# Kernel optimization log

Measured on AMD Instinct MI355X. Metric: run time of the kernel, lower is better.

Reference implementation:

```python
import jax, jax.numpy as jnp
import numpy as np

K_TOP = 2  # top-k experts per token


def setup_inputs() -> dict:
    key = jax.random.key(0)
    k1, k2, k3 = jax.random.split(key, 3)
    B, S, H, E = 4, 2048, 1024, 8
    hidden_states = jax.random.normal(k1, (B, S, H), dtype=jnp.float32)
    router_w = jax.random.normal(k2, (E, H), dtype=jnp.float32) * 0.02
    expert_weights = jax.random.normal(k3, (E, H, H), dtype=jnp.float32) * 0.02
    return {"hidden_states": hidden_states, "router_w": router_w, "expert_weights": expert_weights}


def reference(hidden_states, router_w, expert_weights):
    B, S, H = hidden_states.shape
    x = hidden_states.reshape(-1, H)                      # [N, H], N = B*S
    logits = x @ router_w.T                               # [N, E]
    probs = jax.nn.softmax(logits, axis=-1)               # [N, E]
    topk_vals, topk_idx = jax.lax.top_k(probs, K_TOP)     # [N, K]
    topk_w = topk_vals / (topk_vals.sum(-1, keepdims=True) + 1e-6)  # [N, K]

    # Dense per-expert GEMM over all tokens (single-device dispatch = identity)
    expert_out = jnp.einsum('nh,eho->eno', x, expert_weights)  # [E, N, H]

    # all_to_all_combine: gather each token's K expert outputs
    combined = jnp.take_along_axis(
        expert_out.transpose(1, 0, 2),                    # [N, E, H]
        topk_idx[:, :, None], axis=1)                     # [N, K, H]
    combined = combined.transpose(1, 0, 2)                # [K, N, H]

    # remap bias: sum over last dim of one-hot(topk_idx) * router_prob == gathered prob
    remap_bias = jnp.take_along_axis(probs, topk_idx, axis=1).T[:, :, None]  # [K, N, 1]

    weights = topk_w.T[:, :, None]                        # [K, N, 1]
    out = ((combined + remap_bias) * weights).sum(axis=0) # [N, H]
    return out.reshape(B, S, H)
```

## Files before the change

### kernel.cpp

```cpp
#include <hip/hip_runtime.h>
#include <cstdint>

typedef unsigned short u16;
typedef __attribute__((ext_vector_type(8))) short short8;
typedef __attribute__((ext_vector_type(4))) float float4v;

#define NTOK 8192
#define HDIM 1024
#define NEXP 8
#define TM 128
#define TN 128
#define BK 32
#define MAXT 136

__device__ __forceinline__ u16 f2bf(float f) {
    union { float f; uint32_t u; } v; v.f = f;
    uint32_t u = v.u;
    return (u16)((u + 0x7FFFu + ((u >> 16) & 1u)) >> 16);
}

__device__ __forceinline__ void gll16(const u16* g, u16* l) {
    __builtin_amdgcn_global_load_lds(
        (const __attribute__((address_space(1))) uint32_t*)g,
        (__attribute__((address_space(3))) uint32_t*)l,
        16, 0, 0);
}

__global__ __launch_bounds__(256) void prep_w(const float* __restrict__ w,
                                              u16* __restrict__ wt) {
    __shared__ float tile[32][33];
    const int e  = blockIdx.z;
    const int k0 = blockIdx.x * 32;
    const int n0 = blockIdx.y * 32;
    const int r = threadIdx.x >> 3;
    const int c = (threadIdx.x & 7) * 4;
    const float4 v = *(const float4*)(w + ((size_t)e << 20) + (size_t)(k0 + r) * HDIM + n0 + c);
    tile[r][c] = v.x; tile[r][c+1] = v.y; tile[r][c+2] = v.z; tile[r][c+3] = v.w;
    __syncthreads();
    ushort4 o;
    o.x = f2bf(tile[c][r]); o.y = f2bf(tile[c+1][r]);
    o.z = f2bf(tile[c+2][r]); o.w = f2bf(tile[c+3][r]);
    *(ushort4*)(wt + ((size_t)e << 20) + (size_t)(n0 + r) * HDIM + k0 + c) = o;
}

__global__ __launch_bounds__(256) void router(const float* __restrict__ x,
                                              const float* __restrict__ rw,
                                              u16* __restrict__ x_bf,
                                              float* __restrict__ wt0,
                                              float* __restrict__ wt1,
                                              float* __restrict__ biasv,
                                              int* __restrict__ sel) {
    const int wv = threadIdx.x >> 6;
    const int l  = threadIdx.x & 63;
    const int n  = blockIdx.x * 4 + wv;
    const float4* xr = (const float4*)(x + (size_t)n * HDIM);
    ushort4* xo = (ushort4*)(x_bf + (size_t)n * HDIM);

    float4 xv[4];
#pragma unroll
    for (int t = 0; t < 4; t++) {
        xv[t] = xr[t * 64 + l];
        ushort4 p;
        p.x = f2bf(xv[t].x); p.y = f2bf(xv[t].y);
        p.z = f2bf(xv[t].z); p.w = f2bf(xv[t].w);
        xo[t * 64 + l] = p;
    }

    float logits[NEXP];
#pragma unroll
    for (int e = 0; e < NEXP; e++) {
        const float4* rwe = (const float4*)(rw + e * HDIM);
        float acc = 0.f;
#pragma unroll
        for (int t = 0; t < 4; t++) {
            const float4 r = rwe[t * 64 + l];
            acc += xv[t].x * r.x + xv[t].y * r.y + xv[t].z * r.z + xv[t].w * r.w;
        }
#pragma unroll
        for (int s = 32; s > 0; s >>= 1) acc += __shfl_xor(acc, s, 64);
        logits[e] = acc;
    }

    if (l == 0) {
        float mx = logits[0];
#pragma unroll
        for (int e = 1; e < NEXP; e++) mx = fmaxf(mx, logits[e]);
        float p[NEXP]; float sum = 0.f;
#pragma unroll
        for (int e = 0; e < NEXP; e++) { p[e] = expf(logits[e] - mx); sum += p[e]; }
        const float inv = 1.f / sum;
#pragma unroll
        for (int e = 0; e < NEXP; e++) p[e] *= inv;
        int e0 = 0;
#pragma unroll
        for (int e = 1; e < NEXP; e++) if (p[e] > p[e0]) e0 = e;
        int e1 = (e0 == 0) ? 1 : 0;
#pragma unroll
        for (int e = 0; e < NEXP; e++) if (e != e0 && p[e] > p[e1]) e1 = e;
        const float p0 = p[e0], p1 = p[e1];
        const float wsum = p0 + p1 + 1e-6f;
        const float w0 = p0 / wsum, w1 = p1 / wsum;
        wt0[n] = w0; wt1[n] = w1;
        biasv[n] = w0 * p0 + w1 * p1;
        sel[n] = e0 | (e1 << 8);
    }
}

__global__ __launch_bounds__(256) void build_lists(const int* __restrict__ sel,
                                                   int* __restrict__ lists,
                                                   int* __restrict__ counts) {
    const int n  = blockIdx.x * 256 + threadIdx.x;
    const int wv = threadIdx.x >> 6;
    const int l  = threadIdx.x & 63;
    const int s  = sel[n];
    const int e0 = s & 0xFF, e1 = s >> 8;
    __shared__ int wcnt[NEXP][4];
    __shared__ int ebase[NEXP];
    int pf0 = 0, pf1 = 0;
    const unsigned long long ltmask = (1ULL << l) - 1ULL;
#pragma unroll
    for (int e = 0; e < NEXP; e++) {
        const int slot = (e0 == e) ? 0 : ((e1 == e) ? 1 : -1);
        const unsigned long long bal = __ballot(slot >= 0);
        const int pf = __popcll(bal & ltmask);
        if (slot == 0) pf0 = pf;
        if (slot == 1) pf1 = pf;
        if (l == 0) wcnt[e][wv] = __popcll(bal);
    }
    __syncthreads();
    if (threadIdx.x < NEXP) {
        const int e = threadIdx.x;
        const int tot = wcnt[e][0] + wcnt[e][1] + wcnt[e][2] + wcnt[e][3];
        ebase[e] = atomicAdd(&counts[e * 16], tot);
    }
    __syncthreads();
    int off0 = ebase[e0], off1 = ebase[e1];
#pragma unroll
    for (int i = 0; i < 4; i++) {
        off0 += (i < wv) ? wcnt[e0][i] : 0;
        off1 += (i < wv) ? wcnt[e1][i] : 0;
    }
    lists[e0 * NTOK + off0 + pf0] = n;
    lists[e1 * NTOK + off1 + pf1] = n | 0x10000;
}

__global__ __launch_bounds__(64) void plan_tiles(const int* __restrict__ counts,
                                                 int* __restrict__ tmap) {
    if (threadIdx.x == 0) {
        int idx = 0;
        for (int e = 0; e < NEXP; e++) {
            const int nt = (counts[e * 16] + TM - 1) / TM;
            for (int m = 0; m < nt; m++) tmap[idx++] = (e << 16) | m;
        }
        for (int i = idx; i < MAXT; i++) tmap[i] = -1;
    }
}

__global__ __launch_bounds__(256) void moe_gemm(const u16* __restrict__ x_bf,
                                                const u16* __restrict__ wt_bf,
                                                const int* __restrict__ lists,
                                                const int* __restrict__ counts,
                                                const int* __restrict__ tmap,
                                                const float* __restrict__ wt0,
                                                const float* __restrict__ wt1,
                                                const float* __restrict__ biasv,
                                                float* __restrict__ out) {
    const int ent = tmap[blockIdx.x];
    if (ent < 0) return;
    const int e = ent >> 16;
    const int tile_m = (ent & 0xFFFF) * TM;
    const int cnt = counts[e * 16];
    const int tn = blockIdx.y * TN;

    __shared__ u16 lA[TM * BK];
    __shared__ u16 lB[TN * BK];
    __shared__ int   toks[TM];
    __shared__ float wgt[TM];
    __shared__ float bia[TM];

    const int t  = threadIdx.x;
    const int wv = t >> 6;
    const int l  = t & 63;

    if (t < TM) {
        const int idx = tile_m + t;
        int tok = 0; float w = 0.f, b = 0.f;
        if (idx < cnt) {
            const int entry = lists[e * NTOK + idx];
            tok = entry & 0xFFFF;
            const int slot = entry >> 16;
            w = slot ? wt1[tok] : wt0[tok];
            b = slot ? 0.f : biasv[tok];
        }
        toks[t] = tok; wgt[t] = w; bia[t] = b;
    }
    __syncthreads();

    const int c0 = wv * 2, c1 = wv * 2 + 1;
    const int rs0 = c0 * 16 + (l >> 2);
    const int rs1 = c1 * 16 + (l >> 2);
    const int koff = (l & 3) * 8;
    const u16* pA0 = x_bf + (size_t)toks[rs0] * HDIM + koff;
    const u16* pA1 = x_bf + (size_t)toks[rs1] * HDIM + koff;
    const u16* pB0 = wt_bf + ((size_t)e << 20) + (size_t)(tn + rs0) * HDIM + koff;
    const u16* pB1 = wt_bf + ((size_t)e << 20) + (size_t)(tn + rs1) * HDIM + koff;
    u16* qA0 = lA + c0 * 512;
    u16* qA1 = lA + c1 * 512;
    u16* qB0 = lB + c0 * 512;
    u16* qB1 = lB + c1 * 512;

    const int wm = (wv & 1) * 64;
    const int wn = (wv >> 1) * 64;
    const int fm = l & 15;
    const int fk = (l >> 4) * 8;

    float4v acc[4][4];
#pragma unroll
    for (int i = 0; i < 4; i++)
#pragma unroll
        for (int j = 0; j < 4; j++) { float4v z = {0.f, 0.f, 0.f, 0.f}; acc[i][j] = z; }

    for (int k0 = 0; k0 < HDIM; k0 += BK) {
        __syncthreads();
        gll16(pA0 + k0, qA0);
        gll16(pA1 + k0, qA1);
        gll16(pB0 + k0, qB0);
        gll16(pB1 + k0, qB1);
        __syncthreads();

        short8 af[4], bf[4];
#pragma unroll
        for (int mf = 0; mf < 4; mf++)
            af[mf] = *(const short8*)&lA[(wm + mf * 16 + fm) * BK + fk];
#pragma unroll
        for (int nf = 0; nf < 4; nf++)
            bf[nf] = *(const short8*)&lB[(wn + nf * 16 + fm) * BK + fk];
#pragma unroll
        for (int mf = 0; mf < 4; mf++)
#pragma unroll
            for (int nf = 0; nf < 4; nf++)
                acc[mf][nf] = __builtin_amdgcn_mfma_f32_16x16x32_bf16(af[mf], bf[nf], acc[mf][nf], 0, 0, 0);
    }

#pragma unroll
    for (int mf = 0; mf < 4; mf++) {
#pragma unroll
        for (int r = 0; r < 4; r++) {
            const int m_local = wm + mf * 16 + (l >> 4) * 4 + r;
            if (tile_m + m_local < cnt) {
                const int tok = toks[m_local];
                const float w = wgt[m_local], b = bia[m_local];
#pragma unroll
                for (int nf = 0; nf < 4; nf++) {
                    const int h = tn + wn + nf * 16 + fm;
                    atomicAdd(&out[(size_t)tok * HDIM + h], acc[mf][nf][r] * w + b);
                }
            }
        }
    }
}

extern "C" void kernel_launch(void* const* d_in, const int* in_sizes, int n_in,
                              void* d_out, int out_size, void* d_ws, size_t ws_size,
                              hipStream_t stream) {
    const float* x  = (const float*)d_in[0];
    const float* rw = (const float*)d_in[1];
    const float* ew = (const float*)d_in[2];
    float* out = (float*)d_out;

    char* ws = (char*)d_ws;
    u16*   x_bf   = (u16*)ws;
    u16*   w_bf   = (u16*)(ws + 16777216);
    float* wt0    = (float*)(ws + 33554432);
    float* wt1    = (float*)(ws + 33587200);
    float* biasv  = (float*)(ws + 33619968);
    int*   sel    = (int*)(ws + 33652736);
    int*   lists  = (int*)(ws + 33685504);
    int*   counts = (int*)(ws + 33947648);
    int*   tmap   = (int*)(ws + 33948160);

    hipMemsetAsync(d_out, 0, (size_t)out_size * sizeof(float), stream);
    hipMemsetAsync(counts, 0, NEXP * 16 * sizeof(int), stream);

    prep_w<<<dim3(32, 32, NEXP), 256, 0, stream>>>(ew, w_bf);
    router<<<NTOK / 4, 256, 0, stream>>>(x, rw, x_bf, wt0, wt1, biasv, sel);
    build_lists<<<NTOK / 256, 256, 0, stream>>>(sel, lists, counts);
    plan_tiles<<<1, 64, 0, stream>>>(counts, tmap);
    moe_gemm<<<dim3(MAXT, HDIM / TN, 1), 256, 0, stream>>>(
        x_bf, w_bf, lists, counts, tmap, wt0, wt1, biasv, out);
}
```

Baseline: 230.3 us.

## Replace atomic output with fp16 per-slot staging, combine kernel, BK=64 swizzled LDS

The GEMM epilogue no longer does float atomicAdd into a zeroed output. Each token-slot result is stored as fp16 into one of two staging buffers, and a new combine kernel sums them into the output, which removes the output memset and the atomic traffic. The K tile is doubled to 64 and LDS rows are XOR-swizzled to avoid bank conflicts while halving the number of barriers. The cost is an extra kernel pass over two 16MB staging buffers and a loss of precision from fp16 storage.

```diff
diff --git a/kernel.cpp b/kernel.cpp
--- a/kernel.cpp
+++ b/kernel.cpp
@@ -1,4 +1,5 @@
 #include <hip/hip_runtime.h>
+#include <hip/hip_fp16.h>
 #include <cstdint>
 
 typedef unsigned short u16;
@@ -10,7 +11,7 @@
 #define NEXP 8
 #define TM 128
 #define TN 128
-#define BK 32
+#define BK 64
 #define MAXT 136
 
 __device__ __forceinline__ u16 f2bf(float f) {
@@ -164,7 +165,8 @@
                                                 const float* __restrict__ wt0,
                                                 const float* __restrict__ wt1,
                                                 const float* __restrict__ biasv,
-                                                float* __restrict__ out) {
+                                                __half* __restrict__ stage0,
+                                                __half* __restrict__ stage1) {
     const int ent = tmap[blockIdx.x];
     if (ent < 0) return;
     const int e = ent >> 16;
@@ -177,6 +179,7 @@
     __shared__ int   toks[TM];
     __shared__ float wgt[TM];
     __shared__ float bia[TM];
+    __shared__ int   slt[TM];
 
     const int t  = threadIdx.x;
     const int wv = t >> 6;
@@ -184,35 +187,43 @@
 
     if (t < TM) {
         const int idx = tile_m + t;
-        int tok = 0; float w = 0.f, b = 0.f;
+        int tok = 0; float w = 0.f, b = 0.f; int sl = 0;
         if (idx < cnt) {
             const int entry = lists[e * NTOK + idx];
             tok = entry & 0xFFFF;
-            const int slot = entry >> 16;
-            w = slot ? wt1[tok] : wt0[tok];
-            b = slot ? 0.f : biasv[tok];
-        }
-        toks[t] = tok; wgt[t] = w; bia[t] = b;
+            sl = entry >> 16;
+            w = sl ? wt1[tok] : wt0[tok];
+            b = sl ? 0.f : biasv[tok];
+        }
+        toks[t] = tok; wgt[t] = w; bia[t] = b; slt[t] = sl;
     }
     __syncthreads();
 
-    const int c0 = wv * 2, c1 = wv * 2 + 1;
-    const int rs0 = c0 * 16 + (l >> 2);
-    const int rs1 = c1 * 16 + (l >> 2);
-    const int koff = (l & 3) * 8;
-    const u16* pA0 = x_bf + (size_t)toks[rs0] * HDIM + koff;
-    const u16* pA1 = x_bf + (size_t)toks[rs1] * HDIM + koff;
-    const u16* pB0 = wt_bf + ((size_t)e << 20) + (size_t)(tn + rs0) * HDIM + koff;
-    const u16* pB1 = wt_bf + ((size_t)e << 20) + (size_t)(tn + rs1) * HDIM + koff;
-    u16* qA0 = lA + c0 * 512;
-    u16* qA1 = lA + c1 * 512;
-    u16* qB0 = lB + c0 * 512;
-    u16* qB1 = lB + c1 * 512;
+    const int r_in = l >> 3;
+    const int koff = (((l & 7) ^ r_in)) * 8;
+    const u16* pA[4]; const u16* pB[4]; u16* qA[4]; u16* qB[4];
+#pragma unroll
+    for (int i = 0; i < 4; i++) {
+        const int c = wv * 4 + i;
+        const int row = c * 8 + r_in;
+        pA[i] = x_bf + (size_t)toks[row] * HDIM + koff;
+        pB[i] = wt_bf + ((size_t)e << 20) + (size_t)(tn + row) * HDIM + koff;
+        qA[i] = lA + c * 512;
+        qB[i] = lB + c * 512;
+    }
 
     const int wm = (wv & 1) * 64;
     const int wn = (wv >> 1) * 64;
     const int fm = l & 15;
-    const int fk = (l >> 4) * 8;
+    const int fq = l >> 4;
+    int aoff[4], boff[4];
+#pragma unroll
+    for (int i = 0; i < 4; i++) {
+        const int ra = wm + i * 16 + fm;
+        const int rb = wn + i * 16 + fm;
+        aoff[i] = ra * 64 + ((fq ^ (ra & 7)) * 8);
+        boff[i] = rb * 64 + ((fq ^ (rb & 7)) * 8);
+    }
 
     float4v acc[4][4];
 #pragma unroll
@@ -222,42 +233,67 @@
 
     for (int k0 = 0; k0 < HDIM; k0 += BK) {
         __syncthreads();
-        gll16(pA0 + k0, qA0);
-        gll16(pA1 + k0, qA1);
-        gll16(pB0 + k0, qB0);
-        gll16(pB1 + k0, qB1);
+#pragma unroll
+        for (int i = 0; i < 4; i++) {
+            gll16(pA[i] + k0, qA[i]);
+            gll16(pB[i] + k0, qB[i]);
+        }
         __syncthreads();
 
-        short8 af[4], bf[4];
-#pragma unroll
-        for (int mf = 0; mf < 4; mf++)
-            af[mf] = *(const short8*)&lA[(wm + mf * 16 + fm) * BK + fk];
-#pragma unroll
-        for (int nf = 0; nf < 4; nf++)
-            bf[nf] = *(const short8*)&lB[(wn + nf * 16 + fm) * BK + fk];
-#pragma unroll
-        for (int mf = 0; mf < 4; mf++)
+#pragma unroll
+        for (int kh = 0; kh < 2; kh++) {
+            short8 af[4], bf[4];
+#pragma unroll
+            for (int mf = 0; mf < 4; mf++)
+                af[mf] = *(const short8*)&lA[aoff[mf] ^ (kh << 5)];
 #pragma unroll
             for (int nf = 0; nf < 4; nf++)
-                acc[mf][nf] = __builtin_amdgcn_mfma_f32_16x16x32_bf16(af[mf], bf[nf], acc[mf][nf], 0, 0, 0);
+                bf[nf] = *(const short8*)&lB[boff[nf] ^ (kh << 5)];
+#pragma unroll
+            for (int mf = 0; mf < 4; mf++)
+#pragma unroll
+                for (int nf = 0; nf < 4; nf++)
+                    acc[mf][nf] = __builtin_amdgcn_mfma_f32_16x16x32_bf16(af[mf], bf[nf], acc[mf][nf], 0, 0, 0);
+        }
     }
 
 #pragma unroll
     for (int mf = 0; mf < 4; mf++) {
 #pragma unroll
         for (int r = 0; r < 4; r++) {
-            const int m_local = wm + mf * 16 + (l >> 4) * 4 + r;
+            const int m_local = wm + mf * 16 + fq * 4 + r;
             if (tile_m + m_local < cnt) {
                 const int tok = toks[m_local];
                 const float w = wgt[m_local], b = bia[m_local];
+                __half* sp = (slt[m_local] ? stage1 : stage0) + (size_t)tok * HDIM;
 #pragma unroll
                 for (int nf = 0; nf < 4; nf++) {
                     const int h = tn + wn + nf * 16 + fm;
-                    atomicAdd(&out[(size_t)tok * HDIM + h], acc[mf][nf][r] * w + b);
+                    sp[h] = __float2half(acc[mf][nf][r] * w + b);
                 }
             }
         }
     }
+}
+
+__global__ __launch_bounds__(256) void combine(const __half* __restrict__ s0,
+                                               const __half* __restrict__ s1,
+                                               float* __restrict__ out) {
+    const size_t idx = ((size_t)blockIdx.x * 256 + threadIdx.x) * 8;
+    union { uint4 v; __half h[8]; } a, b;
+    a.v = *(const uint4*)(s0 + idx);
+    b.v = *(const uint4*)(s1 + idx);
+    float4 o0, o1;
+    o0.x = __half2float(a.h[0]) + __half2float(b.h[0]);
+    o0.y = __half2float(a.h[1]) + __half2float(b.h[1]);
+    o0.z = __half2float(a.h[2]) + __half2float(b.h[2]);
+    o0.w = __half2float(a.h[3]) + __half2float(b.h[3]);
+    o1.x = __half2float(a.h[4]) + __half2float(b.h[4]);
+    o1.y = __half2float(a.h[5]) + __half2float(b.h[5]);
+    o1.z = __half2float(a.h[6]) + __half2float(b.h[6]);
+    o1.w = __half2float(a.h[7]) + __half2float(b.h[7]);
+    *(float4*)(out + idx)     = o0;
+    *(float4*)(out + idx + 4) = o1;
 }
 
 extern "C" void kernel_launch(void* const* d_in, const int* in_sizes, int n_in,
@@ -269,17 +305,18 @@
     float* out = (float*)d_out;
 
     char* ws = (char*)d_ws;
-    u16*   x_bf   = (u16*)ws;
-    u16*   w_bf   = (u16*)(ws + 16777216);
-    float* wt0    = (float*)(ws + 33554432);
-    float* wt1    = (float*)(ws + 33587200);
-    float* biasv  = (float*)(ws + 33619968);
-    int*   sel    = (int*)(ws + 33652736);
-    int*   lists  = (int*)(ws + 33685504);
-    int*   counts = (int*)(ws + 33947648);
-    int*   tmap   = (int*)(ws + 33948160);
-
-    hipMemsetAsync(d_out, 0, (size_t)out_size * sizeof(float), stream);
+    u16*    x_bf   = (u16*)ws;
+    u16*    w_bf   = (u16*)(ws + 16777216);
+    __half* stage0 = (__half*)(ws + 33554432);
+    __half* stage1 = (__half*)(ws + 50331648);
+    float*  wt0    = (float*)(ws + 67108864);
+    float*  wt1    = (float*)(ws + 67141632);
+    float*  biasv  = (float*)(ws + 67174400);
+    int*    sel    = (int*)(ws + 67207168);
+    int*    lists  = (int*)(ws + 67239936);
+    int*    counts = (int*)(ws + 67502080);
+    int*    tmap   = (int*)(ws + 67502592);
+
     hipMemsetAsync(counts, 0, NEXP * 16 * sizeof(int), stream);
 
     prep_w<<<dim3(32, 32, NEXP), 256, 0, stream>>>(ew, w_bf);
@@ -287,5 +324,6 @@
     build_lists<<<NTOK / 256, 256, 0, stream>>>(sel, lists, counts);
     plan_tiles<<<1, 64, 0, stream>>>(counts, tmap);
     moe_gemm<<<dim3(MAXT, HDIM / TN, 1), 256, 0, stream>>>(
-        x_bf, w_bf, lists, counts, tmap, wt0, wt1, biasv, out);
-}
+        x_bf, w_bf, lists, counts, tmap, wt0, wt1, biasv, stage0, stage1);
+    combine<<<(NTOK * HDIM) / (256 * 8), 256, 0, stream>>>(stage0, stage1, out);
+}
```

After: 200.6 us. 12.9% less time.
